# Performance work log

Measured on AMD Instinct MI355X. Metric: run time of the kernel, lower is better.

## Reference

```python
import jax, jax.numpy as jnp
import numpy as np

H, NOPE, ROPE, VD, KV_LORA, HID = 16, 128, 64, 128, 512, 2048
QK = NOPE + ROPE
SCALE = QK ** -0.5
EPS = 1e-5


def _rope(x, freqs):
    # x: [b, t, h, ROPE]; freqs: [t, ROPE//2] angles. Complex-pair rotation.
    cos = jnp.cos(freqs)[None, :, None, :]
    sin = jnp.sin(freqs)[None, :, None, :]
    xr = x.reshape(x.shape[:-1] + (ROPE // 2, 2))
    x1, x2 = xr[..., 0], xr[..., 1]
    o1 = x1 * cos - x2 * sin
    o2 = x1 * sin + x2 * cos
    return jnp.stack([o1, o2], axis=-1).reshape(x.shape)


def _layernorm(x, g, b):
    mu = jnp.mean(x, axis=-1, keepdims=True)
    var = jnp.var(x, axis=-1, keepdims=True)
    return (x - mu) * jax.lax.rsqrt(var + EPS) * g + b


def setup_inputs() -> dict:
    key = jax.random.key(0)
    ks = jax.random.split(key, 6)
    b, t = 2, 2048

    def xavier(k, shape):
        fan_in, fan_out = shape
        lim = np.sqrt(6.0 / (fan_in + fan_out))
        return jax.random.uniform(k, shape, jnp.float32, -lim, lim)

    hidden_states = jax.random.normal(ks[0], (b, t, HID), jnp.float32)
    # rope angles: theta_i = 10000^(-2i/ROPE), angle[p,i] = p * theta_i
    inv_freq = 1.0 / (10000.0 ** (np.arange(0, ROPE, 2, dtype=np.float32) / ROPE))
    freqs = jnp.asarray(np.arange(t, dtype=np.float32)[:, None] * inv_freq[None, :])
    # causal additive mask broadcastable to [b,t,s,h]
    causal = jnp.where(jnp.arange(t)[None, :] <= jnp.arange(t)[:, None], 0.0, -1e9)
    attention_mask = causal.astype(jnp.float32)[None, :, :, None]
    return {
        "hidden_states": hidden_states,
        "freqs": freqs,
        "attention_mask": attention_mask,
        "Wq": xavier(ks[1], (HID, H * QK)),
        "Wkv_a": xavier(ks[2], (HID, KV_LORA + ROPE)),
        "kv_gamma": jnp.ones((KV_LORA,), jnp.float32),
        "kv_beta": jnp.zeros((KV_LORA,), jnp.float32),
        "Wkv_b": xavier(ks[3], (KV_LORA, H * (NOPE + VD))),
        "Wout": xavier(ks[4], (H * VD, HID)),
    }


def reference(hidden_states, freqs, attention_mask, Wq, Wkv_a, kv_gamma, kv_beta, Wkv_b, Wout):
    b, t, _ = hidden_states.shape
    # Q projection -> [b,t,H,QK], split nope/rope, rotate rope part
    q = (hidden_states @ Wq).reshape(b, t, H, QK)
    q_nope, q_rope = q[..., :NOPE], q[..., NOPE:]
    q_rope = _rope(q_rope, freqs)
    # compressed KV latent + shared rope key
    kv = hidden_states @ Wkv_a                      # [b,t,KV_LORA+ROPE]
    kv_lat, k_rope = kv[..., :KV_LORA], kv[..., KV_LORA:]
    k_rope = _rope(k_rope[:, :, None, :], freqs)    # [b,t,1,ROPE]
    kv_lat = _layernorm(kv_lat, kv_gamma, kv_beta)
    kvb = (kv_lat @ Wkv_b).reshape(b, t, H, NOPE + VD)
    k_nope, v = kvb[..., :NOPE], kvb[..., NOPE:]
    k = jnp.concatenate([k_nope, jnp.broadcast_to(k_rope, (b, t, H, ROPE))], axis=-1)
    q = jnp.concatenate([q_nope, q_rope], axis=-1)
    # scores [b,t,s,h]; NOTE: source applies softmax over dim=-1 == HEAD axis (faithful)
    scores = jnp.einsum("bthd,bshd->btsh", q, k) * SCALE + attention_mask
    weights = jax.nn.softmax(scores.astype(jnp.float32), axis=-1).astype(q.dtype)
    attn = jnp.einsum("btsh,bshd->bthd", weights, v).reshape(b, t, H * VD)
    return attn @ Wout
```

## Files before the change

kernel.cpp:

```cpp
#include <hip/hip_runtime.h>

typedef unsigned short u16;
typedef short bf16x8 __attribute__((ext_vector_type(8)));
typedef float f32x4 __attribute__((ext_vector_type(4)));
typedef unsigned short u16x8 __attribute__((ext_vector_type(8)));

#define GLOBAL_AS __attribute__((address_space(1)))
#define LDS_AS __attribute__((address_space(3)))
#define DEVINL __device__ __forceinline__

#define BATCH 2
#define TSEQ 2048
#define NHEAD 16
#define QK 192
#define VD 128
#define HID 2048
#define MROWS 4096
#define SCALE_QK 0.07216878364870323f

DEVINL float b2f(u16 u) { union { unsigned i; float f; } x; x.i = ((unsigned)u) << 16; return x.f; }
DEVINL u16 f2b(float f) {
    union { float f; unsigned u; } x; x.f = f;
    unsigned r = x.u + 0x7fffu + ((x.u >> 16) & 1u);
    return (u16)(r >> 16);
}
DEVINL void gload_lds16(const u16* g, u16* l) {
    __builtin_amdgcn_global_load_lds((const GLOBAL_AS unsigned*)g, (LDS_AS unsigned*)l, 16, 0, 0);
}


__global__ void cvt_bf16x8(const float* __restrict__ in, u16* __restrict__ out, int n8) {
    int i = blockIdx.x * 256 + threadIdx.x;
    if (i < n8) {
        const float4* p = (const float4*)(in + (size_t)i * 8);
        float4 x = p[0], y = p[1];
        u16x8 o;
        o[0] = f2b(x.x); o[1] = f2b(x.y); o[2] = f2b(x.z); o[3] = f2b(x.w);
        o[4] = f2b(y.x); o[5] = f2b(y.y); o[6] = f2b(y.z); o[7] = f2b(y.w);
        *(u16x8*)(out + (size_t)i * 8) = o;
    }
}

__global__ void rope_tab_k(const float* __restrict__ freqs, float2* __restrict__ tab) {
    int i = blockIdx.x * 256 + threadIdx.x;
    float f = freqs[i], s, c;
    sincosf(f, &s, &c);
    tab[i] = make_float2(c, s);
}

__global__ void transpose_cvt(const float* __restrict__ in, u16* __restrict__ out,
                              int R, int C, int Cpad) {
    __shared__ float tile[32][33];
    int c0 = blockIdx.x * 32, r0 = blockIdx.y * 32;
    int tx = threadIdx.x, ty = threadIdx.y;
#pragma unroll
    for (int j = 0; j < 4; j++) {
        int r = r0 + ty + j * 8, c = c0 + tx;
        tile[ty + j * 8][tx] = (c < C) ? in[(size_t)r * C + c] : 0.f;
    }
    __syncthreads();
#pragma unroll
    for (int j = 0; j < 4; j++) {
        int oc = c0 + ty + j * 8;
        int orr = r0 + tx;
        if (oc < Cpad) out[(size_t)oc * R + orr] = f2b(tile[tx][ty + j * 8]);
    }
}

template<int MODE>
__global__ __launch_bounds__(256)
void gemm_bt(const u16* __restrict__ A, const u16* __restrict__ BT, int Kdim,
             void* __restrict__ out0, void* __restrict__ out1) {
    __shared__ __align__(16) u16 As[128 * 32];
    __shared__ __align__(16) u16 Bs[128 * 32];
    const int tid = threadIdx.x, lane = tid & 63, wave = tid >> 6;
    const int m0 = blockIdx.x * 128, n0 = blockIdx.y * 128;
    const int wr = wave >> 1, wc = wave & 1;

    f32x4 acc[4][4];
#pragma unroll
    for (int i = 0; i < 4; i++)
#pragma unroll
        for (int j = 0; j < 4; j++) acc[i][j] = f32x4{0.f, 0.f, 0.f, 0.f};

    const int e0 = (wave * 2 + 0) * 512 + lane * 8;
    const int e1 = (wave * 2 + 1) * 512 + lane * 8;
    const u16* gA0 = A + (size_t)(m0 + (e0 >> 5)) * Kdim + (e0 & 31);
    const u16* gA1 = A + (size_t)(m0 + (e1 >> 5)) * Kdim + (e1 & 31);
    const u16* gB0 = BT + (size_t)(n0 + (e0 >> 5)) * Kdim + (e0 & 31);
    const u16* gB1 = BT + (size_t)(n0 + (e1 >> 5)) * Kdim + (e1 & 31);
    u16* lA0 = &As[(wave * 2 + 0) * 512];
    u16* lA1 = &As[(wave * 2 + 1) * 512];
    u16* lB0 = &Bs[(wave * 2 + 0) * 512];
    u16* lB1 = &Bs[(wave * 2 + 1) * 512];

    const int arow = lane & 15, koff = (lane >> 4) * 8;

    for (int k0 = 0; k0 < Kdim; k0 += 32) {
        gload_lds16(gA0, lA0); gload_lds16(gA1, lA1);
        gload_lds16(gB0, lB0); gload_lds16(gB1, lB1);
        gA0 += 32; gA1 += 32; gB0 += 32; gB1 += 32;
        asm volatile("s_waitcnt vmcnt(0)" ::: "memory");
        __syncthreads();
        bf16x8 af[4], bfr[4];
#pragma unroll
        for (int i = 0; i < 4; i++)
            af[i] = *(const bf16x8*)&As[(wr * 64 + i * 16 + arow) * 32 + koff];
#pragma unroll
        for (int j = 0; j < 4; j++)
            bfr[j] = *(const bf16x8*)&Bs[(wc * 64 + j * 16 + arow) * 32 + koff];
#pragma unroll
        for (int i = 0; i < 4; i++)
#pragma unroll
            for (int j = 0; j < 4; j++)
                acc[i][j] = __builtin_amdgcn_mfma_f32_16x16x32_bf16(af[i], bfr[j], acc[i][j], 0, 0, 0);
        __syncthreads();
    }

#pragma unroll
    for (int i = 0; i < 4; i++)
#pragma unroll
        for (int j = 0; j < 4; j++)
#pragma unroll
            for (int r = 0; r < 4; r++) {
                int row = m0 + wr * 64 + i * 16 + (lane >> 4) * 4 + r;
                int col = n0 + wc * 64 + j * 16 + (lane & 15);
                float v = acc[i][j][r];
                if constexpr (MODE == 0) {
                    int h = col / 192, d = col % 192;
                    int b = row >> 11, t = row & 2047;
                    ((u16*)out0)[((size_t)(b * 16 + h) * 2048 + t) * 192 + d] = f2b(v);
                } else if constexpr (MODE == 1) {
                    ((float*)out0)[(size_t)row * 640 + col] = v;
                } else if constexpr (MODE == 2) {
                    int h = col >> 8, d = col & 255;
                    int b = row >> 11, t = row & 2047;
                    size_t base = (size_t)(b * 16 + h) * 2048 + t;
                    if (d < 128) ((u16*)out0)[base * 192 + d] = f2b(v);
                    else         ((u16*)out1)[base * 128 + (d - 128)] = f2b(v);
                } else {
                    ((float*)out0)[(size_t)row * 2048 + col] = v;
                }
            }
}

__global__ __launch_bounds__(256)
void ln_krope(const float* __restrict__ kvf, const float* __restrict__ gamma,
              const float* __restrict__ beta, const float2* __restrict__ tab,
              u16* __restrict__ kvlat, u16* __restrict__ kbuf) {
    int row = blockIdx.x, tid = threadIdx.x;
    const float* x = kvf + (size_t)row * 640;
    float v0 = x[tid], v1 = x[tid + 256];
    float s = v0 + v1, sq = v0 * v0 + v1 * v1;
#pragma unroll
    for (int off = 1; off < 64; off <<= 1) { s += __shfl_xor(s, off); sq += __shfl_xor(sq, off); }
    __shared__ float ssum[4], ssq[4];
    if ((tid & 63) == 0) { ssum[tid >> 6] = s; ssq[tid >> 6] = sq; }
    __syncthreads();
    s = ssum[0] + ssum[1] + ssum[2] + ssum[3];
    sq = ssq[0] + ssq[1] + ssq[2] + ssq[3];
    float mu = s * (1.f / 512.f);
    float var = sq * (1.f / 512.f) - mu * mu;
    float rs = rsqrtf(var + 1e-5f);
    kvlat[(size_t)row * 512 + tid] = f2b((v0 - mu) * rs * gamma[tid] + beta[tid]);
    kvlat[(size_t)row * 512 + tid + 256] = f2b((v1 - mu) * rs * gamma[tid + 256] + beta[tid + 256]);
    if (tid < 32) {
        int t = row & 2047, b = row >> 11;
        float x1 = x[512 + 2 * tid], x2 = x[512 + 2 * tid + 1];
        float2 cs = tab[t * 32 + tid];
        u16 u1 = f2b(x1 * cs.x - x2 * cs.y), u2 = f2b(x1 * cs.y + x2 * cs.x);
        for (int h = 0; h < 16; ++h) {
            size_t base = ((size_t)(b * 16 + h) * 2048 + t) * 192 + 128 + 2 * tid;
            kbuf[base] = u1; kbuf[base + 1] = u2;
        }
    }
}

__global__ void q_rope(u16* __restrict__ qbuf, const float2* __restrict__ tab) {
    int gid = blockIdx.x * 256 + threadIdx.x;
    int g = gid & 7, t = (gid >> 3) & 2047, bh = gid >> 14;
    size_t base = ((size_t)bh * 2048 + t) * 192 + 128 + g * 8;
    u16x8 v = *(u16x8*)(qbuf + base);
    u16x8 o;
#pragma unroll
    for (int k = 0; k < 4; k++) {
        float2 cs = tab[t * 32 + g * 4 + k];
        float x1 = b2f(v[2 * k]), x2 = b2f(v[2 * k + 1]);
        o[2 * k] = f2b(x1 * cs.x - x2 * cs.y);
        o[2 * k + 1] = f2b(x1 * cs.y + x2 * cs.x);
    }
    *(u16x8*)(qbuf + base) = o;
}

__global__ __launch_bounds__(256)
void transpose_v(const u16* __restrict__ vbuf, u16* __restrict__ vtbuf) {
    __shared__ __align__(16) u16 st[64 * 128];
    const int tid = threadIdx.x;
    const int bh = blockIdx.x, t0 = blockIdx.y * 64;
#pragma unroll
    for (int j = 0; j < 4; j++) {
        int c1 = tid + j * 256;
        int t = c1 >> 4, cc = c1 & 15;
        int cs = cc ^ (t & 7) ^ ((t >> 3) & 7);
        bf16x8 v = *(const bf16x8*)(vbuf + ((size_t)bh * 2048 + t0 + t) * 128 + cc * 8);
        *(bf16x8*)&st[t * 128 + cs * 8] = v;
    }
    __syncthreads();
#pragma unroll
    for (int j = 0; j < 4; j++) {
        int c2 = tid + j * 256;
        int d = c2 >> 3, tc8 = (c2 & 7) * 8;
        u16x8 ov;
#pragma unroll
        for (int k2 = 0; k2 < 8; k2++) {
            int t = tc8 + k2;
            int cs = (d >> 3) ^ (t & 7) ^ ((t >> 3) & 7);
            ov[k2] = st[t * 128 + cs * 8 + (d & 7)];
        }
        *(u16x8*)(vtbuf + ((size_t)bh * 128 + d) * 2048 + t0 + tc8) = ov;
    }
}

__global__ void suff1(const u16* __restrict__ vbuf, float* __restrict__ psum) {
    int bh = blockIdx.x, c = blockIdx.y, d = threadIdx.x;
    float s = 0.f;
    const u16* vp = vbuf + ((size_t)bh * 2048 + c * 128) * 128 + d;
    for (int tt = 0; tt < 128; ++tt) s += b2f(vp[(size_t)tt * 128]);
    psum[((size_t)bh * 16 + c) * 128 + d] = s;
}
__global__ void suff2(const float* __restrict__ psum, float* __restrict__ csuf) {
    int bh = blockIdx.x, d = threadIdx.x;
    float run = 0.f;
    for (int c = 15; c >= 0; --c) {
        csuf[((size_t)bh * 16 + c) * 128 + d] = run;
        run += psum[((size_t)bh * 16 + c) * 128 + d];
    }
}
__global__ void suff3(const u16* __restrict__ vbuf, const float* __restrict__ csuf,
                      u16* __restrict__ attnb) {
    int bh = blockIdx.x, c = blockIdx.y, d = threadIdx.x;
    int b = bh >> 4, h = bh & 15;
    float run = csuf[((size_t)bh * 16 + c) * 128 + d];
    for (int tt = 127; tt >= 0; --tt) {
        int t = c * 128 + tt;
        attnb[((size_t)b * 2048 + t) * 2048 + h * 128 + d] = f2b(run * 0.0625f);
        run += b2f(vbuf[((size_t)bh * 2048 + t) * 128 + d]);
    }
}

__global__ __launch_bounds__(256, 3)
void z_kernel(const u16* __restrict__ qbuf, const u16* __restrict__ kbuf,
              u16* __restrict__ zbuf) {
    __shared__ __align__(16) u16 Ks[2][64 * 192];
    const int tid = threadIdx.x, lane = tid & 63, wave = tid >> 6;
    int id = blockIdx.x;
    int b = id & 1, p = id >> 1;
    int tT = (int)((sqrtf(8.f * (float)p + 1.f) - 1.f) * 0.5f);
    while ((tT + 1) * (tT + 2) / 2 <= p) ++tT;
    while (tT * (tT + 1) / 2 > p) --tT;
    int sT = p - tT * (tT + 1) / 2;
    const int t0 = tT * 64, s0 = sT * 64;
    const int col = lane & 15, koff8 = (lane >> 4) * 8, rowb = (lane >> 4) * 4;
    const int qrow = t0 + wave * 16 + col;

    f32x4 zacc[4];
#pragma unroll
    for (int n = 0; n < 4; n++) zacc[n] = f32x4{0.f, 0.f, 0.f, 0.f};

    auto QLOAD = [&](int h, bf16x8 (&q)[6]) {
        const u16* qp = qbuf + ((size_t)(b * 16 + h) * 2048 + qrow) * 192 + koff8;
#pragma unroll
        for (int kk = 0; kk < 6; kk++) q[kk] = *(const bf16x8*)(qp + kk * 32);
    };
    auto KSTAGE = [&](int h, int bi) {
        const size_t hrow = (size_t)(b * 16 + h) * 2048;
#pragma unroll
        for (int j = 0; j < 6; j++) {
            int cidx = (wave * 6 + j) * 64 + lane;
            int rr2 = cidx / 24, cc = cidx % 24, cs = cc ^ (rr2 & 7);
            gload_lds16(kbuf + (hrow + s0 + rr2) * 192 + cs * 8, &Ks[bi][cidx * 8]);
        }
    };
    auto COMPUTE = [&](const bf16x8 (&q)[6], const u16* K) {
        f32x4 e[4];
#pragma unroll
        for (int n = 0; n < 4; n++) e[n] = f32x4{0.f, 0.f, 0.f, 0.f};
#pragma unroll
        for (int kk = 0; kk < 6; kk++) {
            int ca = kk * 4 + (lane >> 4);
#pragma unroll
            for (int n = 0; n < 4; n++) {
                int br = n * 16 + col;
                bf16x8 kf = *(const bf16x8*)&K[br * 192 + ((ca ^ (br & 7)) * 8)];
                e[n] = __builtin_amdgcn_mfma_f32_16x16x32_bf16(q[kk], kf, e[n], 0, 0, 0);
            }
        }
#pragma unroll
        for (int n = 0; n < 4; n++)
#pragma unroll
            for (int r = 0; r < 4; r++)
                zacc[n][r] += __expf(e[n][r] * SCALE_QK);
    };

    bf16x8 qA[6], qB[6];
    QLOAD(0, qA);
    KSTAGE(0, 0);
    for (int hh = 0; hh < 8; ++hh) {
        int h0 = hh * 2;
        QLOAD(h0 + 1, qB);
        KSTAGE(h0 + 1, 1);
        asm volatile("s_waitcnt vmcnt(12)" ::: "memory");
        __builtin_amdgcn_s_barrier();
        __builtin_amdgcn_sched_barrier(0);
        COMPUTE(qA, &Ks[0][0]);
        __builtin_amdgcn_s_barrier();
        if (hh < 7) {
            QLOAD(h0 + 2, qA);
            KSTAGE(h0 + 2, 0);
            asm volatile("s_waitcnt vmcnt(12)" ::: "memory");
        } else {
            asm volatile("s_waitcnt vmcnt(0)" ::: "memory");
        }
        __builtin_amdgcn_s_barrier();
        __builtin_amdgcn_sched_barrier(0);
        COMPUTE(qB, &Ks[1][0]);
        __builtin_amdgcn_s_barrier();
    }
#pragma unroll
    for (int n = 0; n < 4; n++)
#pragma unroll
        for (int r = 0; r < 4; r++) {
            int tg = t0 + wave * 16 + rowb + r, sg = s0 + n * 16 + col;
            zbuf[((size_t)b * 2048 + tg) * 2048 + sg] = f2b(__fdividef(1.f, zacc[n][r]));
        }
}

__global__ __launch_bounds__(512, 2)
void attn_pv(const u16* __restrict__ qbuf, const u16* __restrict__ kbuf,
             const u16* __restrict__ vtbuf, const u16* __restrict__ zbuf,
             u16* __restrict__ attnb) {
    __shared__ __align__(16) u16 Ks[2][64 * 192];
    __shared__ __align__(16) u16 Vt[2][128 * 64];
    __shared__ __align__(16) u16 Zs[2][128 * 64];
    __shared__ __align__(16) u16 Ps[8][16 * 72];
    const int tid = threadIdx.x, lane = tid & 63, wave = tid >> 6;
    int id = blockIdx.x;
    int xcd = id & 7, j2 = id >> 3;
    int pr = j2 & 7, g = j2 >> 3;
    int bh = xcd * 4 + g;
    const int b = bh >> 4, h = bh & 15;
    const int col = lane & 15, koff8 = (lane >> 4) * 8, rowb = (lane >> 4) * 4;
    const size_t kvrow = (size_t)bh * 2048;

    for (int part = 0; part < 2; ++part) {
        const int T = part ? (15 - pr) : pr;
        const int t0 = T * 128, nst = 2 * T + 2;

        bf16x8 qf[6];
        {
            const u16* qp = qbuf + (kvrow + t0 + wave * 16 + col) * 192 + koff8;
#pragma unroll
            for (int kk = 0; kk < 6; kk++) qf[kk] = *(const bf16x8*)(qp + kk * 32);
        }
        f32x4 o[8];
#pragma unroll
        for (int nt = 0; nt < 8; nt++) o[nt] = f32x4{0.f, 0.f, 0.f, 0.f};

        auto STAGE = [&](int st, int bi) {
            const int s0 = st * 64;
#pragma unroll
            for (int j = 0; j < 3; j++) {
                int cidx = (wave * 3 + j) * 64 + lane;
                int rr2 = cidx / 24, cc = cidx % 24, cs = cc ^ (rr2 & 7);
                gload_lds16(kbuf + (kvrow + s0 + rr2) * 192 + cs * 8, &Ks[bi][cidx * 8]);
            }
#pragma unroll
            for (int j = 0; j < 2; j++) {
                int cidx = (wave * 2 + j) * 64 + lane;
                int d = cidx >> 3, cc = cidx & 7, cs = cc ^ (d & 7);
                gload_lds16(vtbuf + ((size_t)bh * 128 + d) * 2048 + s0 + cs * 8, &Vt[bi][cidx * 8]);
            }
#pragma unroll
            for (int j = 0; j < 2; j++) {
                int cidx = (wave * 2 + j) * 64 + lane;
                int zr = cidx >> 3, zc = cidx & 7, zcs = zc ^ (zr & 7);
                gload_lds16(zbuf + ((size_t)b * 2048 + t0 + zr) * 2048 + s0 + zcs * 8, &Zs[bi][cidx * 8]);
            }
        };
        STAGE(0, 0);
        for (int st = 0; st < nst; ++st) {
            int cur = st & 1;
            if (st + 1 < nst) {
                STAGE(st + 1, cur ^ 1);
                asm volatile("s_waitcnt vmcnt(7)" ::: "memory");
            } else {
                asm volatile("s_waitcnt vmcnt(0)" ::: "memory");
            }
            __builtin_amdgcn_s_barrier();
            __builtin_amdgcn_sched_barrier(0);
            const int s0 = st * 64;
            f32x4 sc[4];
#pragma unroll
            for (int n = 0; n < 4; n++) sc[n] = f32x4{0.f, 0.f, 0.f, 0.f};
#pragma unroll
            for (int kk = 0; kk < 6; kk++) {
                int ca = kk * 4 + (lane >> 4);
#pragma unroll
                for (int n = 0; n < 4; n++) {
                    int br = n * 16 + col;
                    bf16x8 kf = *(const bf16x8*)&Ks[cur][br * 192 + ((ca ^ (br & 7)) * 8)];
                    sc[n] = __builtin_amdgcn_mfma_f32_16x16x32_bf16(qf[kk], kf, sc[n], 0, 0, 0);
                }
            }
#pragma unroll
            for (int n = 0; n < 4; n++)
#pragma unroll
                for (int rr = 0; rr < 4; rr++) {
                    int tr = wave * 16 + rowb + rr;
                    int tg = t0 + tr, sg = s0 + n * 16 + col;
                    float w = 0.f;
                    if (sg <= tg) {
                        int sl = n * 16 + col;
                        float rz = b2f(Zs[cur][tr * 64 + (((sl >> 3) ^ (tr & 7)) << 3) + (sl & 7)]);
                        w = __expf(sc[n][rr] * SCALE_QK) * rz;
                    }
                    Ps[wave][(rowb + rr) * 72 + n * 16 + col] = f2b(w);
                }
#pragma unroll
            for (int kk = 0; kk < 2; kk++) {
                bf16x8 pa = *(const bf16x8*)&Ps[wave][col * 72 + kk * 32 + koff8];
                int ca = kk * 4 + (lane >> 4);
#pragma unroll
                for (int nt = 0; nt < 8; nt++) {
                    int d = nt * 16 + col;
                    bf16x8 vb = *(const bf16x8*)&Vt[cur][d * 64 + ((ca ^ (d & 7)) * 8)];
                    o[nt] = __builtin_amdgcn_mfma_f32_16x16x32_bf16(pa, vb, o[nt], 0, 0, 0);
                }
            }
            __builtin_amdgcn_s_barrier();
        }
#pragma unroll
        for (int nt = 0; nt < 8; nt++)
#pragma unroll
            for (int rr = 0; rr < 4; rr++) {
                int t = t0 + wave * 16 + rowb + rr, d = nt * 16 + col;
                size_t oi = ((size_t)b * 2048 + t) * 2048 + h * 128 + d;
                attnb[oi] = f2b(o[nt][rr] + b2f(attnb[oi]));
            }
    }
}

extern "C" void kernel_launch(void* const* d_in, const int* in_sizes, int n_in,
                              void* d_out, int out_size, void* d_ws, size_t ws_size,
                              hipStream_t stream) {
    (void)in_sizes; (void)n_in; (void)out_size;
    const float* hidden = (const float*)d_in[0];
    const float* freqs  = (const float*)d_in[1];
    const float* Wq     = (const float*)d_in[3];
    const float* Wkva   = (const float*)d_in[4];
    const float* gamma  = (const float*)d_in[5];
    const float* beta   = (const float*)d_in[6];
    const float* Wkvb   = (const float*)d_in[7];
    const float* Wout   = (const float*)d_in[8];
    float* outp = (float*)d_out;

    char* ws = (char*)d_ws;
    size_t off = 0;
    auto alloc = [&](size_t bytes) -> void* {
        void* p = ws + off; off += (bytes + 255) & ~(size_t)255; return p;
    };
    u16*   hid_b = (u16*)alloc((size_t)MROWS * HID * 2);
    u16*   WqT   = (u16*)alloc((size_t)3072 * 2048 * 2);
    u16*   WkvaT = (u16*)alloc((size_t)640 * 2048 * 2);
    u16*   WkvbT = (u16*)alloc((size_t)4096 * 512 * 2);
    u16*   WoutT = (u16*)alloc((size_t)2048 * 2048 * 2);
    u16*   qbuf  = (u16*)alloc((size_t)BATCH * NHEAD * TSEQ * QK * 2);
    float* kvf   = (float*)alloc((size_t)MROWS * 640 * 4);
    u16*   kvlat = (u16*)alloc((size_t)MROWS * 512 * 2);
    u16*   kbuf  = (u16*)alloc((size_t)BATCH * NHEAD * TSEQ * QK * 2);
    u16*   vbuf  = (u16*)alloc((size_t)BATCH * NHEAD * TSEQ * VD * 2);
    u16*   attnb = (u16*)alloc((size_t)MROWS * 2048 * 2);
    float2* ropetab = (float2*)alloc((size_t)2048 * 32 * 8);
    float* psum  = (float*)alloc((size_t)32 * 16 * 128 * 4);
    float* csuf  = (float*)alloc((size_t)32 * 16 * 128 * 4);
    if (off > ws_size) return;
    u16* zbuf  = WqT;
    u16* vtbuf = hid_b;

    cvt_bf16x8<<<4096, 256, 0, stream>>>(hidden, hid_b, MROWS * HID / 8);
    rope_tab_k<<<256, 256, 0, stream>>>(freqs, ropetab);
    dim3 tb(32, 8);
    transpose_cvt<<<dim3(96, 64), tb, 0, stream>>>(Wq, WqT, 2048, 3072, 3072);
    transpose_cvt<<<dim3(20, 64), tb, 0, stream>>>(Wkva, WkvaT, 2048, 576, 640);
    transpose_cvt<<<dim3(128, 16), tb, 0, stream>>>(Wkvb, WkvbT, 512, 4096, 4096);
    transpose_cvt<<<dim3(64, 64), tb, 0, stream>>>(Wout, WoutT, 2048, 2048, 2048);

    gemm_bt<1><<<dim3(32, 5), 256, 0, stream>>>(hid_b, WkvaT, 2048, kvf, nullptr);
    ln_krope<<<MROWS, 256, 0, stream>>>(kvf, gamma, beta, ropetab, kvlat, kbuf);
    gemm_bt<2><<<dim3(32, 32), 256, 0, stream>>>(kvlat, WkvbT, 512, kbuf, vbuf);
    gemm_bt<0><<<dim3(32, 24), 256, 0, stream>>>(hid_b, WqT, 2048, qbuf, nullptr);
    q_rope<<<2048, 256, 0, stream>>>(qbuf, ropetab);

    transpose_v<<<dim3(32, 32), 256, 0, stream>>>(vbuf, vtbuf);
    suff1<<<dim3(32, 16), 128, 0, stream>>>(vbuf, psum);
    suff2<<<32, 128, 0, stream>>>(psum, csuf);
    suff3<<<dim3(32, 16), 128, 0, stream>>>(vbuf, csuf, attnb);

    z_kernel<<<1056, 256, 0, stream>>>(qbuf, kbuf, zbuf);
    attn_pv<<<256, 512, 0, stream>>>(qbuf, kbuf, vtbuf, zbuf, attnb);

    gemm_bt<3><<<dim3(32, 16), 256, 0, stream>>>(attnb, WoutT, 2048, outp, nullptr);
}
```

Measured before the change: 439.3 us.

## Switch attention kernels to 32x32 MFMA, fuse q-rope and V transpose into GEMM epilogues

Rewrites z_kernel and attn_pv to use 32x32x16 bf16 MFMA with the K tile as the A operand. Z is stored transposed, the P operand is built in registers with permlane32 swaps instead of an LDS round trip, and the two key-block halves are combined through an LDS reduction. Q RoPE is fused into the Q GEMM epilogue using a lane shuffle, and the V transpose is fused into the KV-b GEMM epilogue, which removes two separate kernels. In exchange, the epilogue writes uncoalesced strided transposed stores, and attn_pv occupancy drops to one block per SM.

```diff
diff --git a/kernel.cpp b/kernel.cpp
--- a/kernel.cpp
+++ b/kernel.cpp
@@ -3,6 +3,7 @@
 typedef unsigned short u16;
 typedef short bf16x8 __attribute__((ext_vector_type(8)));
 typedef float f32x4 __attribute__((ext_vector_type(4)));
+typedef float f32x16 __attribute__((ext_vector_type(16)));
 typedef unsigned short u16x8 __attribute__((ext_vector_type(8)));
 
 #define GLOBAL_AS __attribute__((address_space(1)))
@@ -26,6 +27,11 @@
 }
 DEVINL void gload_lds16(const u16* g, u16* l) {
     __builtin_amdgcn_global_load_lds((const GLOBAL_AS unsigned*)g, (LDS_AS unsigned*)l, 16, 0, 0);
+}
+DEVINL unsigned pk2(float a, float b) {
+    unsigned d;
+    asm("v_cvt_pk_bf16_f32 %0, %1, %2" : "=v"(d) : "v"(a), "v"(b));
+    return d;
 }
 
 
@@ -70,7 +76,8 @@
 template<int MODE>
 __global__ __launch_bounds__(256)
 void gemm_bt(const u16* __restrict__ A, const u16* __restrict__ BT, int Kdim,
-             void* __restrict__ out0, void* __restrict__ out1) {
+             void* __restrict__ out0, void* __restrict__ out1, void* __restrict__ out2,
+             const float2* __restrict__ tab) {
     __shared__ __align__(16) u16 As[128 * 32];
     __shared__ __align__(16) u16 Bs[128 * 32];
     const int tid = threadIdx.x, lane = tid & 63, wave = tid >> 6;
@@ -129,7 +136,13 @@
                 if constexpr (MODE == 0) {
                     int h = col / 192, d = col % 192;
                     int b = row >> 11, t = row & 2047;
-                    ((u16*)out0)[((size_t)(b * 16 + h) * 2048 + t) * 192 + d] = f2b(v);
+                    float vv = v;
+                    float pv = __shfl_xor(v, 1);
+                    if (d >= 128) {
+                        float2 cs = tab[t * 32 + ((d - 128) >> 1)];
+                        vv = v * cs.x + pv * ((lane & 1) ? cs.y : -cs.y);
+                    }
+                    ((u16*)out0)[((size_t)(b * 16 + h) * 2048 + t) * 192 + d] = f2b(vv);
                 } else if constexpr (MODE == 1) {
                     ((float*)out0)[(size_t)row * 640 + col] = v;
                 } else if constexpr (MODE == 2) {
@@ -137,7 +150,11 @@
                     int b = row >> 11, t = row & 2047;
                     size_t base = (size_t)(b * 16 + h) * 2048 + t;
                     if (d < 128) ((u16*)out0)[base * 192 + d] = f2b(v);
-                    else         ((u16*)out1)[base * 128 + (d - 128)] = f2b(v);
+                    else {
+                        u16 bv = f2b(v);
+                        ((u16*)out1)[base * 128 + (d - 128)] = bv;
+                        ((u16*)out2)[((size_t)(b * 16 + h) * 128 + (d - 128)) * 2048 + t] = bv;
+                    }
                 } else {
                     ((float*)out0)[(size_t)row * 2048 + col] = v;
                 }
@@ -176,51 +193,6 @@
     }
 }
 
-__global__ void q_rope(u16* __restrict__ qbuf, const float2* __restrict__ tab) {
-    int gid = blockIdx.x * 256 + threadIdx.x;
-    int g = gid & 7, t = (gid >> 3) & 2047, bh = gid >> 14;
-    size_t base = ((size_t)bh * 2048 + t) * 192 + 128 + g * 8;
-    u16x8 v = *(u16x8*)(qbuf + base);
-    u16x8 o;
-#pragma unroll
-    for (int k = 0; k < 4; k++) {
-        float2 cs = tab[t * 32 + g * 4 + k];
-        float x1 = b2f(v[2 * k]), x2 = b2f(v[2 * k + 1]);
-        o[2 * k] = f2b(x1 * cs.x - x2 * cs.y);
-        o[2 * k + 1] = f2b(x1 * cs.y + x2 * cs.x);
-    }
-    *(u16x8*)(qbuf + base) = o;
-}
-
-__global__ __launch_bounds__(256)
-void transpose_v(const u16* __restrict__ vbuf, u16* __restrict__ vtbuf) {
-    __shared__ __align__(16) u16 st[64 * 128];
-    const int tid = threadIdx.x;
-    const int bh = blockIdx.x, t0 = blockIdx.y * 64;
-#pragma unroll
-    for (int j = 0; j < 4; j++) {
-        int c1 = tid + j * 256;
-        int t = c1 >> 4, cc = c1 & 15;
-        int cs = cc ^ (t & 7) ^ ((t >> 3) & 7);
-        bf16x8 v = *(const bf16x8*)(vbuf + ((size_t)bh * 2048 + t0 + t) * 128 + cc * 8);
-        *(bf16x8*)&st[t * 128 + cs * 8] = v;
-    }
-    __syncthreads();
-#pragma unroll
-    for (int j = 0; j < 4; j++) {
-        int c2 = tid + j * 256;
-        int d = c2 >> 3, tc8 = (c2 & 7) * 8;
-        u16x8 ov;
-#pragma unroll
-        for (int k2 = 0; k2 < 8; k2++) {
-            int t = tc8 + k2;
-            int cs = (d >> 3) ^ (t & 7) ^ ((t >> 3) & 7);
-            ov[k2] = st[t * 128 + cs * 8 + (d & 7)];
-        }
-        *(u16x8*)(vtbuf + ((size_t)bh * 128 + d) * 2048 + t0 + tc8) = ov;
-    }
-}
-
 __global__ void suff1(const u16* __restrict__ vbuf, float* __restrict__ psum) {
     int bh = blockIdx.x, c = blockIdx.y, d = threadIdx.x;
     float s = 0.f;
@@ -250,9 +222,11 @@
 
 __global__ __launch_bounds__(256, 3)
 void z_kernel(const u16* __restrict__ qbuf, const u16* __restrict__ kbuf,
-              u16* __restrict__ zbuf) {
-    __shared__ __align__(16) u16 Ks[2][64 * 192];
+              u16* __restrict__ zbufT) {
+    __shared__ __align__(16) u16 Ks[2 * 12288];
     const int tid = threadIdx.x, lane = tid & 63, wave = tid >> 6;
+    const int hi = lane >> 5, l31 = lane & 31;
+    const int tgrp = wave & 1, sblk = wave >> 1;
     int id = blockIdx.x;
     int b = id & 1, p = id >> 1;
     int tT = (int)((sqrtf(8.f * (float)p + 1.f) - 1.f) * 0.5f);
@@ -260,131 +234,132 @@
     while (tT * (tT + 1) / 2 > p) --tT;
     int sT = p - tT * (tT + 1) / 2;
     const int t0 = tT * 64, s0 = sT * 64;
-    const int col = lane & 15, koff8 = (lane >> 4) * 8, rowb = (lane >> 4) * 4;
-    const int qrow = t0 + wave * 16 + col;
-
-    f32x4 zacc[4];
-#pragma unroll
-    for (int n = 0; n < 4; n++) zacc[n] = f32x4{0.f, 0.f, 0.f, 0.f};
-
-    auto QLOAD = [&](int h, bf16x8 (&q)[6]) {
-        const u16* qp = qbuf + ((size_t)(b * 16 + h) * 2048 + qrow) * 192 + koff8;
-#pragma unroll
-        for (int kk = 0; kk < 6; kk++) q[kk] = *(const bf16x8*)(qp + kk * 32);
+    const int rK = sblk * 32 + l31;
+    const int t_loc = tgrp * 32 + l31;
+
+    float zacc[16];
+#pragma unroll
+    for (int r = 0; r < 16; r++) zacc[r] = 0.f;
+
+    auto QLOAD = [&](int h, bf16x8 (&q)[12]) {
+        const u16* qp = qbuf + ((size_t)(b * 16 + h) * 2048 + t0 + t_loc) * 192 + hi * 8;
+#pragma unroll
+        for (int kk = 0; kk < 12; kk++) q[kk] = *(const bf16x8*)(qp + kk * 16);
     };
     auto KSTAGE = [&](int h, int bi) {
         const size_t hrow = (size_t)(b * 16 + h) * 2048;
 #pragma unroll
         for (int j = 0; j < 6; j++) {
-            int cidx = (wave * 6 + j) * 64 + lane;
-            int rr2 = cidx / 24, cc = cidx % 24, cs = cc ^ (rr2 & 7);
-            gload_lds16(kbuf + (hrow + s0 + rr2) * 192 + cs * 8, &Ks[bi][cidx * 8]);
+            int idx = (wave * 6 + j) * 64 + lane;
+            int rr2 = idx / 24, cc = idx % 24, cs = cc ^ (rr2 & 7);
+            gload_lds16(kbuf + (hrow + s0 + rr2) * 192 + cs * 8, &Ks[bi * 12288 + idx * 8]);
         }
     };
-    auto COMPUTE = [&](const bf16x8 (&q)[6], const u16* K) {
-        f32x4 e[4];
-#pragma unroll
-        for (int n = 0; n < 4; n++) e[n] = f32x4{0.f, 0.f, 0.f, 0.f};
-#pragma unroll
-        for (int kk = 0; kk < 6; kk++) {
-            int ca = kk * 4 + (lane >> 4);
-#pragma unroll
-            for (int n = 0; n < 4; n++) {
-                int br = n * 16 + col;
-                bf16x8 kf = *(const bf16x8*)&K[br * 192 + ((ca ^ (br & 7)) * 8)];
-                e[n] = __builtin_amdgcn_mfma_f32_16x16x32_bf16(q[kk], kf, e[n], 0, 0, 0);
-            }
-        }
-#pragma unroll
-        for (int n = 0; n < 4; n++)
-#pragma unroll
-            for (int r = 0; r < 4; r++)
-                zacc[n][r] += __expf(e[n][r] * SCALE_QK);
+    auto COMPUTE = [&](const bf16x8 (&q)[12], const u16* K) {
+        f32x16 e;
+#pragma unroll
+        for (int r = 0; r < 16; r++) e[r] = 0.f;
+        __builtin_amdgcn_s_setprio(1);
+#pragma unroll
+        for (int kk = 0; kk < 12; kk++) {
+            int slot = (2 * kk + hi) ^ (rK & 7);
+            bf16x8 kf = *(const bf16x8*)&K[rK * 192 + slot * 8];
+            e = __builtin_amdgcn_mfma_f32_32x32x16_bf16(kf, q[kk], e, 0, 0, 0);
+        }
+        __builtin_amdgcn_s_setprio(0);
+#pragma unroll
+        for (int r = 0; r < 16; r++) zacc[r] += __expf(e[r] * SCALE_QK);
     };
 
-    bf16x8 qA[6], qB[6];
+    bf16x8 qA[12], qB[12];
     QLOAD(0, qA);
     KSTAGE(0, 0);
     for (int hh = 0; hh < 8; ++hh) {
         int h0 = hh * 2;
         QLOAD(h0 + 1, qB);
         KSTAGE(h0 + 1, 1);
-        asm volatile("s_waitcnt vmcnt(12)" ::: "memory");
+        asm volatile("s_waitcnt vmcnt(18)" ::: "memory");
         __builtin_amdgcn_s_barrier();
         __builtin_amdgcn_sched_barrier(0);
-        COMPUTE(qA, &Ks[0][0]);
+        COMPUTE(qA, &Ks[0]);
         __builtin_amdgcn_s_barrier();
         if (hh < 7) {
             QLOAD(h0 + 2, qA);
             KSTAGE(h0 + 2, 0);
-            asm volatile("s_waitcnt vmcnt(12)" ::: "memory");
+            asm volatile("s_waitcnt vmcnt(18)" ::: "memory");
         } else {
             asm volatile("s_waitcnt vmcnt(0)" ::: "memory");
         }
         __builtin_amdgcn_s_barrier();
         __builtin_amdgcn_sched_barrier(0);
-        COMPUTE(qB, &Ks[1][0]);
+        COMPUTE(qB, &Ks[12288]);
         __builtin_amdgcn_s_barrier();
     }
 #pragma unroll
-    for (int n = 0; n < 4; n++)
-#pragma unroll
-        for (int r = 0; r < 4; r++) {
-            int tg = t0 + wave * 16 + rowb + r, sg = s0 + n * 16 + col;
-            zbuf[((size_t)b * 2048 + tg) * 2048 + sg] = f2b(__fdividef(1.f, zacc[n][r]));
-        }
-}
-
-__global__ __launch_bounds__(512, 2)
+    for (int r = 0; r < 16; r++) {
+        int spat = (r & 3) + 8 * (r >> 2) + 4 * hi;
+        int sg = s0 + sblk * 32 + spat;
+        zbufT[((size_t)b * 2048 + sg) * 2048 + t0 + t_loc] = f2b(__fdividef(1.f, zacc[r]));
+    }
+}
+
+__global__ __launch_bounds__(512, 1)
 void attn_pv(const u16* __restrict__ qbuf, const u16* __restrict__ kbuf,
-             const u16* __restrict__ vtbuf, const u16* __restrict__ zbuf,
+             const u16* __restrict__ vtbuf, const u16* __restrict__ zbufT,
              u16* __restrict__ attnb) {
-    __shared__ __align__(16) u16 Ks[2][64 * 192];
-    __shared__ __align__(16) u16 Vt[2][128 * 64];
-    __shared__ __align__(16) u16 Zs[2][128 * 64];
-    __shared__ __align__(16) u16 Ps[8][16 * 72];
+    __shared__ __align__(16) u16 lds[57344];
+    u16* Ks = lds;
+    u16* Vt = lds + 24576;
+    u16* Zs = lds + 40960;
     const int tid = threadIdx.x, lane = tid & 63, wave = tid >> 6;
+    const int hi = lane >> 5, l31 = lane & 31;
+    const int tgrp = wave & 3, sblk = wave >> 2;
     int id = blockIdx.x;
     int xcd = id & 7, j2 = id >> 3;
     int pr = j2 & 7, g = j2 >> 3;
     int bh = xcd * 4 + g;
     const int b = bh >> 4, h = bh & 15;
-    const int col = lane & 15, koff8 = (lane >> 4) * 8, rowb = (lane >> 4) * 4;
     const size_t kvrow = (size_t)bh * 2048;
+    const int rK = sblk * 32 + l31;
+    const int t_loc = tgrp * 32 + l31;
+    const int zg = t_loc >> 3, zoff = t_loc & 7;
 
     for (int part = 0; part < 2; ++part) {
         const int T = part ? (15 - pr) : pr;
-        const int t0 = T * 128, nst = 2 * T + 2;
-
-        bf16x8 qf[6];
+        const int t0p = T * 128, nst = 2 * T + 2;
+        const int tg = t0p + t_loc;
+
+        bf16x8 qf[12];
         {
-            const u16* qp = qbuf + (kvrow + t0 + wave * 16 + col) * 192 + koff8;
-#pragma unroll
-            for (int kk = 0; kk < 6; kk++) qf[kk] = *(const bf16x8*)(qp + kk * 32);
-        }
-        f32x4 o[8];
-#pragma unroll
-        for (int nt = 0; nt < 8; nt++) o[nt] = f32x4{0.f, 0.f, 0.f, 0.f};
+            const u16* qp = qbuf + (kvrow + tg) * 192 + hi * 8;
+#pragma unroll
+            for (int kk = 0; kk < 12; kk++) qf[kk] = *(const bf16x8*)(qp + kk * 16);
+        }
+        f32x16 o[4];
+#pragma unroll
+        for (int db = 0; db < 4; db++)
+#pragma unroll
+            for (int r = 0; r < 16; r++) o[db][r] = 0.f;
 
         auto STAGE = [&](int st, int bi) {
             const int s0 = st * 64;
 #pragma unroll
             for (int j = 0; j < 3; j++) {
-                int cidx = (wave * 3 + j) * 64 + lane;
-                int rr2 = cidx / 24, cc = cidx % 24, cs = cc ^ (rr2 & 7);
-                gload_lds16(kbuf + (kvrow + s0 + rr2) * 192 + cs * 8, &Ks[bi][cidx * 8]);
+                int idx = (wave * 3 + j) * 64 + lane;
+                int rr2 = idx / 24, cc = idx % 24, cs = cc ^ (rr2 & 7);
+                gload_lds16(kbuf + (kvrow + s0 + rr2) * 192 + cs * 8, &Ks[bi * 12288 + idx * 8]);
             }
 #pragma unroll
             for (int j = 0; j < 2; j++) {
-                int cidx = (wave * 2 + j) * 64 + lane;
-                int d = cidx >> 3, cc = cidx & 7, cs = cc ^ (d & 7);
-                gload_lds16(vtbuf + ((size_t)bh * 128 + d) * 2048 + s0 + cs * 8, &Vt[bi][cidx * 8]);
+                int idx = (wave * 2 + j) * 64 + lane;
+                int d = idx >> 3, cc = idx & 7, cs = cc ^ (d & 7);
+                gload_lds16(vtbuf + ((size_t)bh * 128 + d) * 2048 + s0 + cs * 8, &Vt[bi * 8192 + idx * 8]);
             }
 #pragma unroll
             for (int j = 0; j < 2; j++) {
-                int cidx = (wave * 2 + j) * 64 + lane;
-                int zr = cidx >> 3, zc = cidx & 7, zcs = zc ^ (zr & 7);
-                gload_lds16(zbuf + ((size_t)b * 2048 + t0 + zr) * 2048 + s0 + zcs * 8, &Zs[bi][cidx * 8]);
+                int idx = (wave * 2 + j) * 64 + lane;
+                int sr = idx >> 4, cc = idx & 15, cs = cc ^ (sr & 15);
+                gload_lds16(zbufT + ((size_t)b * 2048 + s0 + sr) * 2048 + t0p + cs * 8, &Zs[bi * 8192 + idx * 8]);
             }
         };
         STAGE(0, 0);
@@ -398,55 +373,79 @@
             }
             __builtin_amdgcn_s_barrier();
             __builtin_amdgcn_sched_barrier(0);
-            const int s0 = st * 64;
-            f32x4 sc[4];
-#pragma unroll
-            for (int n = 0; n < 4; n++) sc[n] = f32x4{0.f, 0.f, 0.f, 0.f};
-#pragma unroll
-            for (int kk = 0; kk < 6; kk++) {
-                int ca = kk * 4 + (lane >> 4);
-#pragma unroll
-                for (int n = 0; n < 4; n++) {
-                    int br = n * 16 + col;
-                    bf16x8 kf = *(const bf16x8*)&Ks[cur][br * 192 + ((ca ^ (br & 7)) * 8)];
-                    sc[n] = __builtin_amdgcn_mfma_f32_16x16x32_bf16(qf[kk], kf, sc[n], 0, 0, 0);
+            const u16* Kc = &Ks[cur * 12288];
+            const u16* Vc = &Vt[cur * 8192];
+            const u16* Zc = &Zs[cur * 8192];
+            f32x16 sacc;
+#pragma unroll
+            for (int r = 0; r < 16; r++) sacc[r] = 0.f;
+            __builtin_amdgcn_s_setprio(1);
+#pragma unroll
+            for (int kk = 0; kk < 12; kk++) {
+                int slot = (2 * kk + hi) ^ (rK & 7);
+                bf16x8 kf = *(const bf16x8*)&Kc[rK * 192 + slot * 8];
+                sacc = __builtin_amdgcn_mfma_f32_32x32x16_bf16(kf, qf[kk], sacc, 0, 0, 0);
+            }
+            __builtin_amdgcn_s_setprio(0);
+            const int s0g = st * 64 + sblk * 32;
+            float w[16];
+#pragma unroll
+            for (int r = 0; r < 16; r++) {
+                int spat = (r & 3) + 8 * (r >> 2) + 4 * hi;
+                int sr = sblk * 32 + spat;
+                float rz = b2f(Zc[sr * 128 + ((zg ^ (sr & 15)) << 3) + zoff]);
+                w[r] = (s0g + spat <= tg) ? __expf(sacc[r] * SCALE_QK) * rz : 0.f;
+            }
+            unsigned pw0 = pk2(w[0], w[1]), pw1 = pk2(w[2], w[3]);
+            unsigned pw2 = pk2(w[4], w[5]), pw3 = pk2(w[6], w[7]);
+            unsigned pw4 = pk2(w[8], w[9]), pw5 = pk2(w[10], w[11]);
+            unsigned pw6 = pk2(w[12], w[13]), pw7 = pk2(w[14], w[15]);
+            unsigned a0 = pw0, a1 = pw1, a2 = pw4, a3 = pw5;
+            asm volatile("v_permlane32_swap_b32 %0, %1" : "+v"(a0), "+v"(pw2));
+            asm volatile("v_permlane32_swap_b32 %0, %1" : "+v"(a1), "+v"(pw3));
+            asm volatile("v_permlane32_swap_b32 %0, %1" : "+v"(a2), "+v"(pw6));
+            asm volatile("v_permlane32_swap_b32 %0, %1" : "+v"(a3), "+v"(pw7));
+            union PU { unsigned u[4]; bf16x8 v; } p0, p1;
+            p0.u[0] = a0;  p0.u[1] = a1;  p0.u[2] = pw2; p0.u[3] = pw3;
+            p1.u[0] = a2;  p1.u[1] = a3;  p1.u[2] = pw6; p1.u[3] = pw7;
+            __builtin_amdgcn_s_setprio(1);
+#pragma unroll
+            for (int db = 0; db < 4; db++) {
+                int dv = db * 32 + l31;
+#pragma unroll
+                for (int ks = 0; ks < 2; ks++) {
+                    int slot = (sblk * 4 + 2 * ks + hi) ^ (dv & 7);
+                    bf16x8 vb = *(const bf16x8*)&Vc[dv * 64 + slot * 8];
+                    o[db] = __builtin_amdgcn_mfma_f32_32x32x16_bf16(ks ? p1.v : p0.v, vb, o[db], 0, 0, 0);
                 }
             }
-#pragma unroll
-            for (int n = 0; n < 4; n++)
-#pragma unroll
-                for (int rr = 0; rr < 4; rr++) {
-                    int tr = wave * 16 + rowb + rr;
-                    int tg = t0 + tr, sg = s0 + n * 16 + col;
-                    float w = 0.f;
-                    if (sg <= tg) {
-                        int sl = n * 16 + col;
-                        float rz = b2f(Zs[cur][tr * 64 + (((sl >> 3) ^ (tr & 7)) << 3) + (sl & 7)]);
-                        w = __expf(sc[n][rr] * SCALE_QK) * rz;
-                    }
-                    Ps[wave][(rowb + rr) * 72 + n * 16 + col] = f2b(w);
+            __builtin_amdgcn_s_setprio(0);
+            __builtin_amdgcn_s_barrier();
+        }
+        __syncthreads();
+        float* red = (float*)lds;
+        if (sblk == 0) {
+#pragma unroll
+            for (int db = 0; db < 4; db++)
+#pragma unroll
+                for (int r = 0; r < 16; r++) {
+                    int trow = (r & 3) + 8 * (r >> 2) + 4 * hi;
+                    red[(tgrp * 32 + trow) * 128 + db * 32 + l31] = o[db][r];
                 }
-#pragma unroll
-            for (int kk = 0; kk < 2; kk++) {
-                bf16x8 pa = *(const bf16x8*)&Ps[wave][col * 72 + kk * 32 + koff8];
-                int ca = kk * 4 + (lane >> 4);
-#pragma unroll
-                for (int nt = 0; nt < 8; nt++) {
-                    int d = nt * 16 + col;
-                    bf16x8 vb = *(const bf16x8*)&Vt[cur][d * 64 + ((ca ^ (d & 7)) * 8)];
-                    o[nt] = __builtin_amdgcn_mfma_f32_16x16x32_bf16(pa, vb, o[nt], 0, 0, 0);
+        }
+        __syncthreads();
+        if (sblk == 1) {
+#pragma unroll
+            for (int db = 0; db < 4; db++)
+#pragma unroll
+                for (int r = 0; r < 16; r++) {
+                    int trow = (r & 3) + 8 * (r >> 2) + 4 * hi;
+                    float val = o[db][r] + red[(tgrp * 32 + trow) * 128 + db * 32 + l31];
+                    size_t oi = ((size_t)b * 2048 + t0p + tgrp * 32 + trow) * 2048 + h * 128 + db * 32 + l31;
+                    attnb[oi] = f2b(val + b2f(attnb[oi]));
                 }
-            }
-            __builtin_amdgcn_s_barrier();
-        }
-#pragma unroll
-        for (int nt = 0; nt < 8; nt++)
-#pragma unroll
-            for (int rr = 0; rr < 4; rr++) {
-                int t = t0 + wave * 16 + rowb + rr, d = nt * 16 + col;
-                size_t oi = ((size_t)b * 2048 + t) * 2048 + h * 128 + d;
-                attnb[oi] = f2b(o[nt][rr] + b2f(attnb[oi]));
-            }
+        }
+        __syncthreads();
     }
 }
 
@@ -484,7 +483,7 @@
     float* psum  = (float*)alloc((size_t)32 * 16 * 128 * 4);
     float* csuf  = (float*)alloc((size_t)32 * 16 * 128 * 4);
     if (off > ws_size) return;
-    u16* zbuf  = WqT;
+    u16* zbufT = WqT;
     u16* vtbuf = hid_b;
 
     cvt_bf16x8<<<4096, 256, 0, stream>>>(hidden, hid_b, MROWS * HID / 8);
@@ -495,19 +494,17 @@
     transpose_cvt<<<dim3(128, 16), tb, 0, stream>>>(Wkvb, WkvbT, 512, 4096, 4096);
     transpose_cvt<<<dim3(64, 64), tb, 0, stream>>>(Wout, WoutT, 2048, 2048, 2048);
 
-    gemm_bt<1><<<dim3(32, 5), 256, 0, stream>>>(hid_b, WkvaT, 2048, kvf, nullptr);
+    gemm_bt<1><<<dim3(32, 5), 256, 0, stream>>>(hid_b, WkvaT, 2048, kvf, nullptr, nullptr, nullptr);
+    gemm_bt<0><<<dim3(32, 24), 256, 0, stream>>>(hid_b, WqT, 2048, qbuf, nullptr, nullptr, ropetab);
     ln_krope<<<MROWS, 256, 0, stream>>>(kvf, gamma, beta, ropetab, kvlat, kbuf);
-    gemm_bt<2><<<dim3(32, 32), 256, 0, stream>>>(kvlat, WkvbT, 512, kbuf, vbuf);
-    gemm_bt<0><<<dim3(32, 24), 256, 0, stream>>>(hid_b, WqT, 2048, qbuf, nullptr);
-    q_rope<<<2048, 256, 0, stream>>>(qbuf, ropetab);
-
-    transpose_v<<<dim3(32, 32), 256, 0, stream>>>(vbuf, vtbuf);
+    gemm_bt<2><<<dim3(32, 32), 256, 0, stream>>>(kvlat, WkvbT, 512, kbuf, vbuf, vtbuf, nullptr);
+
     suff1<<<dim3(32, 16), 128, 0, stream>>>(vbuf, psum);
     suff2<<<32, 128, 0, stream>>>(psum, csuf);
     suff3<<<dim3(32, 16), 128, 0, stream>>>(vbuf, csuf, attnb);
 
-    z_kernel<<<1056, 256, 0, stream>>>(qbuf, kbuf, zbuf);
-    attn_pv<<<256, 512, 0, stream>>>(qbuf, kbuf, vtbuf, zbuf, attnb);
-
-    gemm_bt<3><<<dim3(32, 16), 256, 0, stream>>>(attnb, WoutT, 2048, outp, nullptr);
-}
+    z_kernel<<<1056, 256, 0, stream>>>(qbuf, kbuf, zbufT);
+    attn_pv<<<256, 512, 0, stream>>>(qbuf, kbuf, vtbuf, zbufT, attnb);
+
+    gemm_bt<3><<<dim3(32, 16), 256, 0, stream>>>(attnb, WoutT, 2048, outp, nullptr, nullptr, nullptr);
+}
```

After: 658.6 us. +49.9%, slower.
